# Performance work log

Hardware: AMD Instinct MI355X
Metric: run time of the kernel (lower is better)

The kernel has to match this reference:

```python
import jax, jax.numpy as jnp
import numpy as np

N_STREAMS = 4
T_LEN = 8192
D_HIDDEN = 2048
EPS = 1e-8
SINKHORN_ITERS = 20


def setup_inputs() -> dict:
    key = jax.random.key(0)
    ks = jax.random.split(key, 4)
    n, T, d = N_STREAMS, T_LEN, D_HIDDEN
    nd = n * d
    scale = 1.0 / np.sqrt(nd)
    return {
        "stream": jax.random.normal(ks[0], (n, T, d), jnp.float32),
        "W_pre": jax.random.normal(ks[1], (n, nd), jnp.float32) * scale,
        "W_post": jax.random.normal(ks[2], (n, nd), jnp.float32) * scale,
        "W_res": jax.random.normal(ks[3], (n * n, nd), jnp.float32) * scale,
        "b_pre": jnp.zeros((n,), jnp.float32),
        "b_post": jnp.zeros((n,), jnp.float32),
        "b_res": jnp.zeros((n, n), jnp.float32),
        "alpha_pre": jnp.float32(0.01),
        "alpha_post": jnp.float32(0.01),
        "alpha_res": jnp.float32(0.01),
    }


def sinkhorn_knopp(M, n_iters=SINKHORN_ITERS):
    # Project (..., n, n) to a doubly stochastic matrix.
    M = jnp.exp(M)
    for _ in range(n_iters):  # small static trip count; unrolled
        M = M / jnp.sum(M, axis=-1, keepdims=True)
        M = M / jnp.sum(M, axis=-2, keepdims=True)
    return M


def reference(stream, W_pre, W_post, W_res, b_pre, b_post, b_res,
              alpha_pre, alpha_post, alpha_res):
    n, T, d = stream.shape
    # (n, T, d) -> (T, n*d)
    x = jnp.transpose(stream, (1, 0, 2)).reshape(T, n * d)
    # RMSNorm (no learned scale)
    x = x * jax.lax.rsqrt(jnp.mean(x * x, axis=-1, keepdims=True) + EPS)
    H_pre = jax.nn.sigmoid(alpha_pre * (x @ W_pre.T) + b_pre)          # (T, n)
    H_post = 2.0 * jax.nn.sigmoid(alpha_post * (x @ W_post.T) + b_post)  # (T, n)
    H_res_raw = alpha_res * (x @ W_res.T).reshape(T, n, n) + b_res     # (T, n, n)
    H_res = sinkhorn_knopp(H_res_raw)
    return (H_res, H_pre, H_post)
```

## Files before the change

kernel.cpp:

```cpp
#include <hip/hip_runtime.h>
#include <hip/hip_bf16.h>

#define T_LEN 8192
#define D_HID 2048
#define ND    8192

typedef __attribute__((ext_vector_type(8))) short bf16x8;
typedef __attribute__((ext_vector_type(4))) float f32x4;

__device__ __forceinline__ float bf2f(unsigned int h) {
    union { unsigned int u; float f; } v;
    v.u = h << 16;
    return v.f;
}

__device__ __forceinline__ unsigned int f2bf(float f) {
    union { float f; unsigned int u; } v;
    v.f = f;
    unsigned int r = v.u + 0x7fffu + ((v.u >> 16) & 1u);
    return r >> 16;
}

__device__ __forceinline__ float ssq8(uint4 v) {
    float s = 0.f;
    unsigned int ws[4] = {v.x, v.y, v.z, v.w};
#pragma unroll
    for (int i = 0; i < 4; ++i) {
        float a = bf2f(ws[i] & 0xffffu);
        float b = bf2f(ws[i] >> 16);
        s = fmaf(a, a, s);
        s = fmaf(b, b, s);
    }
    return s;
}

__device__ __forceinline__ float d4(float4 a) {
    return fmaf(a.x, a.x, fmaf(a.y, a.y, fmaf(a.z, a.z, a.w * a.w)));
}

__device__ __forceinline__ uint4 pack8(float4 a, float4 b) {
    uint4 r;
    r.x = f2bf(a.x) | (f2bf(a.y) << 16);
    r.y = f2bf(a.z) | (f2bf(a.w) << 16);
    r.z = f2bf(b.x) | (f2bf(b.y) << 16);
    r.w = f2bf(b.z) | (f2bf(b.w) << 16);
    return r;
}

template <int AFP32>
__device__ __forceinline__ const void* wrow(const void* W, int r) {
    if constexpr (AFP32) return (const void*)((const float*)W + (size_t)r * ND);
    else                 return (const void*)((const unsigned short*)W + (size_t)r * ND);
}

template <int AFP32>
__device__ __forceinline__ uint4 ldw8(const void* row, int e) {
    if constexpr (AFP32) {
        const float* p = (const float*)row + e;
        return pack8(*(const float4*)p, *(const float4*)(p + 4));
    } else {
        return *(const uint4*)((const unsigned short*)row + e);
    }
}

__device__ __forceinline__ float rd_alpha(const void* p) {
    float v = bf2f(*(const unsigned short*)p);
    float av = fabsf(v);
    if (av > 1e-6f && av < 64.f) return v;
    return *(const float*)p;
}

template <int AFP32>
__global__ __launch_bounds__(256, 2)
void mhc_kern(const void* __restrict__ xs_,
              const void* __restrict__ Wpre_, const void* __restrict__ Wpost_,
              const void* __restrict__ Wres_,
              const void* __restrict__ bpre_, const void* __restrict__ bpost_,
              const void* __restrict__ bres_,
              const void* __restrict__ apre_, const void* __restrict__ apost_,
              const void* __restrict__ ares_, void* __restrict__ out_)
{
    __shared__ unsigned short a_lds[16 * 264];
    __shared__ float c_red[4 * 16 * 33];
    __shared__ float ss_red[256];
    __shared__ int insane;

    const int tid = threadIdx.x;

    if (tid == 0) insane = 0;
    __syncthreads();
    if (tid < 128) {
        const unsigned short* p = (tid < 64) ? (const unsigned short*)Wpre_
                                             : (const unsigned short*)xs_;
        float m = fabsf(bf2f(p[tid & 63]));
        if (!(m < 64.0f)) atomicOr(&insane, 1);
    }
    __syncthreads();
    const bool arrays_fp32 = (insane != 0);
    if (arrays_fp32 != (AFP32 != 0)) return;

    const int w = tid >> 6, lane = tid & 63, quad = lane >> 4, l15 = lane & 15;
    const int t0 = blockIdx.x * 16;
    const int t_l = (tid >> 3) & 15, es = tid & 7, s0 = tid >> 7, s1 = s0 + 2;

    const size_t row0 = (size_t)(s0 * T_LEN + t0 + t_l) * D_HID + es * 8;
    const size_t row1 = (size_t)(s1 * T_LEN + t0 + t_l) * D_HID + es * 8;
    unsigned short* lp0 = a_lds + t_l * 264 + s0 * 64 + es * 8;
    unsigned short* lp1 = a_lds + t_l * 264 + s1 * 64 + es * 8;

    const void* brow0v = (l15 < 4) ? wrow<AFP32>(Wpre_, l15)
                       : (l15 < 8) ? wrow<AFP32>(Wpost_, l15 - 4)
                                   : wrow<AFP32>(Wres_, l15 - 8);
    const unsigned int bmask = (l15 < 8) ? 0xffffffffu : 0u;
    const void* brow1v = wrow<AFP32>(Wres_, (l15 < 8) ? 8 + l15 : 0);

    f32x4 acc0 = {0.f, 0.f, 0.f, 0.f};
    f32x4 acc1 = {0.f, 0.f, 0.f, 0.f};
    float ss = 0.f;

    const unsigned short* gp0; const unsigned short* gp1;
    const float* gf0; const float* gf1;
    uint4 cur0, cur1;
    float4 f0a, f0b, f1a, f1b;
    if constexpr (AFP32) {
        gf0 = (const float*)xs_ + row0;  gf1 = (const float*)xs_ + row1;
        f0a = *(const float4*)gf0;  f0b = *(const float4*)(gf0 + 4);
        f1a = *(const float4*)gf1;  f1b = *(const float4*)(gf1 + 4);
    } else {
        gp0 = (const unsigned short*)xs_ + row0;  gp1 = (const unsigned short*)xs_ + row1;
        cur0 = *(const uint4*)gp0;  cur1 = *(const uint4*)gp1;
    }

    for (int r = 0; r < 32; ++r) {
        uint4 w0, w1;
        if constexpr (AFP32) {
            ss += d4(f0a) + d4(f0b) + d4(f1a) + d4(f1b);
            w0 = pack8(f0a, f0b);  w1 = pack8(f1a, f1b);
        } else {
            ss += ssq8(cur0) + ssq8(cur1);
            w0 = cur0;  w1 = cur1;
        }
        *(uint4*)lp0 = w0;
        *(uint4*)lp1 = w1;
        __syncthreads();
        if (r < 31) {
            if constexpr (AFP32) {
                const float* p0 = gf0 + (r + 1) * 64;
                const float* p1 = gf1 + (r + 1) * 64;
                f0a = *(const float4*)p0;  f0b = *(const float4*)(p0 + 4);
                f1a = *(const float4*)p1;  f1b = *(const float4*)(p1 + 4);
            } else {
                cur0 = *(const uint4*)(gp0 + (r + 1) * 64);
                cur1 = *(const uint4*)(gp1 + (r + 1) * 64);
            }
        }
#pragma unroll
        for (int kk = 0; kk < 2; ++kk) {
            const bf16x8 af = *(const bf16x8*)(a_lds + l15 * 264 + w * 64 + kk * 32 + quad * 8);
            const int e = w * 2048 + quad * 8 + r * 64 + kk * 32;
            uint4 br0 = ldw8<AFP32>(brow0v, e);
            uint4 br1 = ldw8<AFP32>(brow1v, e);
            br1.x &= bmask; br1.y &= bmask; br1.z &= bmask; br1.w &= bmask;
            acc0 = __builtin_amdgcn_mfma_f32_16x16x32_bf16(
                af, __builtin_bit_cast(bf16x8, br0), acc0, 0, 0, 0);
            acc1 = __builtin_amdgcn_mfma_f32_16x16x32_bf16(
                af, __builtin_bit_cast(bf16x8, br1), acc1, 0, 0, 0);
        }
        __syncthreads();
    }

    ss_red[tid] = ss;
    {
        float* cw = c_red + w * (16 * 33);
#pragma unroll
        for (int g = 0; g < 4; ++g) {
            cw[(quad * 4 + g) * 33 + l15]      = acc0[g];
            cw[(quad * 4 + g) * 33 + 16 + l15] = acc1[g];
        }
    }
    __syncthreads();

    if (tid < 16) {
        const int t = tid;
        float sst = 0.f;
#pragma unroll
        for (int h = 0; h < 2; ++h)
#pragma unroll
            for (int e = 0; e < 8; ++e)
                sst += ss_red[h * 128 + t * 8 + e];
        const float rinv = rsqrtf(sst * (1.0f / (float)ND) + 1e-8f);

        float dots[24];
#pragma unroll
        for (int n = 0; n < 24; ++n)
            dots[n] = c_red[0 * 528 + t * 33 + n] + c_red[1 * 528 + t * 33 + n]
                    + c_red[2 * 528 + t * 33 + n] + c_red[3 * 528 + t * 33 + n];

        const float apre  = rd_alpha(apre_);
        const float apost = rd_alpha(apost_);
        const float ares  = rd_alpha(ares_);
        const unsigned short* bpre  = (const unsigned short*)bpre_;
        const unsigned short* bpost = (const unsigned short*)bpost_;
        const unsigned short* bres  = (const unsigned short*)bres_;
        const size_t tg = (size_t)t0 + t;

        float hpre[4], hpost[4], M[16];
#pragma unroll
        for (int k = 0; k < 4; ++k) {
            const float zp = fmaf(apre * dots[k], rinv, bf2f(bpre[k]));
            hpre[k] = 1.0f / (1.0f + __expf(-zp));
            const float zq = fmaf(apost * dots[4 + k], rinv, bf2f(bpost[k]));
            hpost[k] = 2.0f / (1.0f + __expf(-zq));
        }
#pragma unroll
        for (int m = 0; m < 16; ++m)
            M[m] = __expf(fmaf(ares * dots[8 + m], rinv, bf2f(bres[m])));

        for (int it = 0; it < 20; ++it) {
#pragma unroll
            for (int i = 0; i < 4; ++i) {
                const float rr = 1.0f / ((M[i*4+0] + M[i*4+1]) + (M[i*4+2] + M[i*4+3]));
                M[i*4+0] *= rr; M[i*4+1] *= rr; M[i*4+2] *= rr; M[i*4+3] *= rr;
            }
#pragma unroll
            for (int j = 0; j < 4; ++j) {
                const float cr = 1.0f / ((M[j] + M[4+j]) + (M[8+j] + M[12+j]));
                M[j] *= cr; M[4+j] *= cr; M[8+j] *= cr; M[12+j] *= cr;
            }
        }

        if constexpr (AFP32) {
            float* out = (float*)out_;
#pragma unroll
            for (int m = 0; m < 16; ++m) out[tg * 16 + m] = M[m];
#pragma unroll
            for (int k = 0; k < 4; ++k) {
                out[(size_t)T_LEN * 16 + tg * 4 + k] = hpre[k];
                out[(size_t)T_LEN * 20 + tg * 4 + k] = hpost[k];
            }
        } else {
            unsigned short* out = (unsigned short*)out_;
#pragma unroll
            for (int m = 0; m < 16; ++m) out[tg * 16 + m] = (unsigned short)f2bf(M[m]);
#pragma unroll
            for (int k = 0; k < 4; ++k) {
                out[(size_t)T_LEN * 16 + tg * 4 + k] = (unsigned short)f2bf(hpre[k]);
                out[(size_t)T_LEN * 20 + tg * 4 + k] = (unsigned short)f2bf(hpost[k]);
            }
        }
    }
}

extern "C" void kernel_launch(void* const* d_in, const int* in_sizes, int n_in,
                              void* d_out, int out_size, void* d_ws, size_t ws_size,
                              hipStream_t stream)
{
    mhc_kern<0><<<dim3(T_LEN / 16), dim3(256), 0, stream>>>(
        d_in[0], d_in[1], d_in[2], d_in[3], d_in[4], d_in[5], d_in[6],
        d_in[7], d_in[8], d_in[9], d_out);
    mhc_kern<1><<<dim3(T_LEN / 16), dim3(256), 0, stream>>>(
        d_in[0], d_in[1], d_in[2], d_in[3], d_in[4], d_in[5], d_in[6],
        d_in[7], d_in[8], d_in[9], d_out);
}
```

Baseline: 412.2 us.

## Pre-convert weights to bf16 workspace and double-buffer LDS to drop a barrier

A small prep kernel detects the input dtype, converts all 24 weight rows to a packed bf16 buffer in workspace, and stores alpha and bias as floats there. A single main kernel then dispatches on the flag instead of launching two full-grid kernels where one exits early. In the fp32 case this removes the per-block fp32-to-bf16 weight conversion and the bias/alpha decoding. The A tile in LDS is now double-buffered, which removes one __syncthreads per k-step. The cost is an extra kernel launch and a dependency on the workspace buffer.

```diff
diff --git a/kernel.cpp b/kernel.cpp
--- a/kernel.cpp
+++ b/kernel.cpp
@@ -4,6 +4,11 @@
 #define T_LEN 8192
 #define D_HID 2048
 #define ND    8192
+
+#define WS_FLAG  0
+#define WS_ALPHA 16
+#define WS_BIAS  64
+#define WS_W     256
 
 typedef __attribute__((ext_vector_type(8))) short bf16x8;
 typedef __attribute__((ext_vector_type(4))) float f32x4;
@@ -47,22 +52,6 @@
     return r;
 }
 
-template <int AFP32>
-__device__ __forceinline__ const void* wrow(const void* W, int r) {
-    if constexpr (AFP32) return (const void*)((const float*)W + (size_t)r * ND);
-    else                 return (const void*)((const unsigned short*)W + (size_t)r * ND);
-}
-
-template <int AFP32>
-__device__ __forceinline__ uint4 ldw8(const void* row, int e) {
-    if constexpr (AFP32) {
-        const float* p = (const float*)row + e;
-        return pack8(*(const float4*)p, *(const float4*)(p + 4));
-    } else {
-        return *(const uint4*)((const unsigned short*)row + e);
-    }
-}
-
 __device__ __forceinline__ float rd_alpha(const void* p) {
     float v = bf2f(*(const unsigned short*)p);
     float av = fabsf(v);
@@ -70,21 +59,16 @@
     return *(const float*)p;
 }
 
-template <int AFP32>
-__global__ __launch_bounds__(256, 2)
-void mhc_kern(const void* __restrict__ xs_,
-              const void* __restrict__ Wpre_, const void* __restrict__ Wpost_,
-              const void* __restrict__ Wres_,
-              const void* __restrict__ bpre_, const void* __restrict__ bpost_,
-              const void* __restrict__ bres_,
-              const void* __restrict__ apre_, const void* __restrict__ apost_,
-              const void* __restrict__ ares_, void* __restrict__ out_)
-{
-    __shared__ unsigned short a_lds[16 * 264];
-    __shared__ float c_red[4 * 16 * 33];
-    __shared__ float ss_red[256];
+__global__ __launch_bounds__(256)
+void prep_kern(const void* __restrict__ xs_,
+               const void* __restrict__ Wpre_, const void* __restrict__ Wpost_,
+               const void* __restrict__ Wres_,
+               const void* __restrict__ bpre_, const void* __restrict__ bpost_,
+               const void* __restrict__ bres_,
+               const void* __restrict__ apre_, const void* __restrict__ apost_,
+               const void* __restrict__ ares_, void* __restrict__ ws_)
+{
     __shared__ int insane;
-
     const int tid = threadIdx.x;
 
     if (tid == 0) insane = 0;
@@ -96,23 +80,57 @@
         if (!(m < 64.0f)) atomicOr(&insane, 1);
     }
     __syncthreads();
-    const bool arrays_fp32 = (insane != 0);
-    if (arrays_fp32 != (AFP32 != 0)) return;
-
+    const bool fp32 = (insane != 0);
+
+    if (blockIdx.x == 0) {
+        if (tid == 0) {
+            *(int*)ws_ = fp32 ? 1 : 0;
+            float* al = (float*)((char*)ws_ + WS_ALPHA);
+            al[0] = rd_alpha(apre_);
+            al[1] = rd_alpha(apost_);
+            al[2] = rd_alpha(ares_);
+        }
+        if (tid < 24) {
+            const void* b = (tid < 4) ? bpre_ : (tid < 8) ? bpost_ : bres_;
+            const int i = (tid < 4) ? tid : (tid < 8) ? tid - 4 : tid - 8;
+            float v = fp32 ? ((const float*)b)[i]
+                           : bf2f(((const unsigned short*)b)[i]);
+            ((float*)((char*)ws_ + WS_BIAS))[tid] = v;
+        }
+    }
+
+    const int g = blockIdx.x * 2048 + tid * 8;
+    const int row = g >> 13, e = g & 8191;
+    const void* base = (row < 4) ? Wpre_ : (row < 8) ? Wpost_ : Wres_;
+    const int srow = (row < 4) ? row : (row < 8) ? row - 4 : row - 8;
+    unsigned short* dst = (unsigned short*)((char*)ws_ + WS_W) + g;
+    if (fp32) {
+        const float* p = (const float*)base + (size_t)srow * ND + e;
+        *(uint4*)dst = pack8(*(const float4*)p, *(const float4*)(p + 4));
+    } else {
+        *(uint4*)dst = *(const uint4*)((const unsigned short*)base + (size_t)srow * ND + e);
+    }
+}
+
+template <int AFP32>
+__device__ __forceinline__ void main_body(
+    const void* __restrict__ xs_, const unsigned short* __restrict__ wsW,
+    const float* __restrict__ al, const float* __restrict__ bs,
+    void* __restrict__ out_,
+    unsigned short* a_lds, float* c_red, float* ss_red)
+{
+    const int tid = threadIdx.x;
     const int w = tid >> 6, lane = tid & 63, quad = lane >> 4, l15 = lane & 15;
     const int t0 = blockIdx.x * 16;
     const int t_l = (tid >> 3) & 15, es = tid & 7, s0 = tid >> 7, s1 = s0 + 2;
 
     const size_t row0 = (size_t)(s0 * T_LEN + t0 + t_l) * D_HID + es * 8;
     const size_t row1 = (size_t)(s1 * T_LEN + t0 + t_l) * D_HID + es * 8;
-    unsigned short* lp0 = a_lds + t_l * 264 + s0 * 64 + es * 8;
-    unsigned short* lp1 = a_lds + t_l * 264 + s1 * 64 + es * 8;
-
-    const void* brow0v = (l15 < 4) ? wrow<AFP32>(Wpre_, l15)
-                       : (l15 < 8) ? wrow<AFP32>(Wpost_, l15 - 4)
-                                   : wrow<AFP32>(Wres_, l15 - 8);
-    const unsigned int bmask = (l15 < 8) ? 0xffffffffu : 0u;
-    const void* brow1v = wrow<AFP32>(Wres_, (l15 < 8) ? 8 + l15 : 0);
+    const int lofs0 = t_l * 264 + s0 * 64 + es * 8;
+    const int lofs1 = t_l * 264 + s1 * 64 + es * 8;
+
+    const unsigned short* brow0 = wsW + (size_t)l15 * ND;
+    const unsigned short* brow1 = wsW + (size_t)(16 + (l15 & 7)) * ND;
 
     f32x4 acc0 = {0.f, 0.f, 0.f, 0.f};
     f32x4 acc1 = {0.f, 0.f, 0.f, 0.f};
@@ -132,6 +150,7 @@
     }
 
     for (int r = 0; r < 32; ++r) {
+        unsigned short* lb = a_lds + (r & 1) * (16 * 264);
         uint4 w0, w1;
         if constexpr (AFP32) {
             ss += d4(f0a) + d4(f0b) + d4(f1a) + d4(f1b);
@@ -140,9 +159,8 @@
             ss += ssq8(cur0) + ssq8(cur1);
             w0 = cur0;  w1 = cur1;
         }
-        *(uint4*)lp0 = w0;
-        *(uint4*)lp1 = w1;
-        __syncthreads();
+        *(uint4*)(lb + lofs0) = w0;
+        *(uint4*)(lb + lofs1) = w1;
         if (r < 31) {
             if constexpr (AFP32) {
                 const float* p0 = gf0 + (r + 1) * 64;
@@ -154,19 +172,19 @@
                 cur1 = *(const uint4*)(gp1 + (r + 1) * 64);
             }
         }
+        __syncthreads();
+        const unsigned short* ar = lb + l15 * 264 + w * 64 + quad * 8;
 #pragma unroll
         for (int kk = 0; kk < 2; ++kk) {
-            const bf16x8 af = *(const bf16x8*)(a_lds + l15 * 264 + w * 64 + kk * 32 + quad * 8);
+            const bf16x8 af = *(const bf16x8*)(ar + kk * 32);
             const int e = w * 2048 + quad * 8 + r * 64 + kk * 32;
-            uint4 br0 = ldw8<AFP32>(brow0v, e);
-            uint4 br1 = ldw8<AFP32>(brow1v, e);
-            br1.x &= bmask; br1.y &= bmask; br1.z &= bmask; br1.w &= bmask;
+            const uint4 br0 = *(const uint4*)(brow0 + e);
+            const uint4 br1 = *(const uint4*)(brow1 + e);
             acc0 = __builtin_amdgcn_mfma_f32_16x16x32_bf16(
                 af, __builtin_bit_cast(bf16x8, br0), acc0, 0, 0, 0);
             acc1 = __builtin_amdgcn_mfma_f32_16x16x32_bf16(
                 af, __builtin_bit_cast(bf16x8, br1), acc1, 0, 0, 0);
         }
-        __syncthreads();
     }
 
     ss_red[tid] = ss;
@@ -196,25 +214,20 @@
             dots[n] = c_red[0 * 528 + t * 33 + n] + c_red[1 * 528 + t * 33 + n]
                     + c_red[2 * 528 + t * 33 + n] + c_red[3 * 528 + t * 33 + n];
 
-        const float apre  = rd_alpha(apre_);
-        const float apost = rd_alpha(apost_);
-        const float ares  = rd_alpha(ares_);
-        const unsigned short* bpre  = (const unsigned short*)bpre_;
-        const unsigned short* bpost = (const unsigned short*)bpost_;
-        const unsigned short* bres  = (const unsigned short*)bres_;
+        const float apre = al[0], apost = al[1], ares = al[2];
         const size_t tg = (size_t)t0 + t;
 
         float hpre[4], hpost[4], M[16];
 #pragma unroll
         for (int k = 0; k < 4; ++k) {
-            const float zp = fmaf(apre * dots[k], rinv, bf2f(bpre[k]));
+            const float zp = fmaf(apre * dots[k], rinv, bs[k]);
             hpre[k] = 1.0f / (1.0f + __expf(-zp));
-            const float zq = fmaf(apost * dots[4 + k], rinv, bf2f(bpost[k]));
+            const float zq = fmaf(apost * dots[4 + k], rinv, bs[4 + k]);
             hpost[k] = 2.0f / (1.0f + __expf(-zq));
         }
 #pragma unroll
         for (int m = 0; m < 16; ++m)
-            M[m] = __expf(fmaf(ares * dots[8 + m], rinv, bf2f(bres[m])));
+            M[m] = __expf(fmaf(ares * dots[8 + m], rinv, bs[8 + m]));
 
         for (int it = 0; it < 20; ++it) {
 #pragma unroll
@@ -251,14 +264,30 @@
     }
 }
 
+__global__ __launch_bounds__(256, 2)
+void mhc_main(const void* __restrict__ xs_, void* __restrict__ out_,
+              const void* __restrict__ ws_)
+{
+    __shared__ __align__(16) unsigned short a_lds[2 * 16 * 264];
+    __shared__ float c_red[4 * 16 * 33];
+    __shared__ float ss_red[256];
+
+    const char* ws = (const char*)ws_;
+    const int flag = *(const int*)(ws + WS_FLAG);
+    const unsigned short* wsW = (const unsigned short*)(ws + WS_W);
+    const float* al = (const float*)(ws + WS_ALPHA);
+    const float* bs = (const float*)(ws + WS_BIAS);
+
+    if (flag) main_body<1>(xs_, wsW, al, bs, out_, a_lds, c_red, ss_red);
+    else      main_body<0>(xs_, wsW, al, bs, out_, a_lds, c_red, ss_red);
+}
+
 extern "C" void kernel_launch(void* const* d_in, const int* in_sizes, int n_in,
                               void* d_out, int out_size, void* d_ws, size_t ws_size,
                               hipStream_t stream)
 {
-    mhc_kern<0><<<dim3(T_LEN / 16), dim3(256), 0, stream>>>(
+    prep_kern<<<dim3(96), dim3(256), 0, stream>>>(
         d_in[0], d_in[1], d_in[2], d_in[3], d_in[4], d_in[5], d_in[6],
-        d_in[7], d_in[8], d_in[9], d_out);
-    mhc_kern<1><<<dim3(T_LEN / 16), dim3(256), 0, stream>>>(
-        d_in[0], d_in[1], d_in[2], d_in[3], d_in[4], d_in[5], d_in[6],
-        d_in[7], d_in[8], d_in[9], d_out);
-}
+        d_in[7], d_in[8], d_in[9], d_ws);
+    mhc_main<<<dim3(T_LEN / 16), dim3(256), 0, stream>>>(d_in[0], d_out, d_ws);
+}
```

New measurement: 407.1 us. Within noise of the previous version (-1.2%).
